# Kernel tuning notes

Measured on AMD Instinct MI355X. Metric: run time of the kernel, lower is better.

Reference implementation:

```python
import jax, jax.numpy as jnp
import numpy as np

B, C, H, W = 4, 512, 64, 64
IC = C // 2  # inter_plane
EPS = 1e-5


def _conv1x1(x, w, b=None):
    # x: [b,c,h,w], w: [o,c] -> [b,o,h,w]
    y = jnp.einsum('bchw,oc->bohw', x, w)
    if b is not None:
        y = y + b[None, :, None, None]
    return y


def setup_inputs() -> dict:
    key = jax.random.key(0)
    ks = jax.random.split(key, 20)
    rn = lambda i, sh, s=0.02: jax.random.normal(ks[i], sh, jnp.float32) * s
    return {
        'xA': jax.random.normal(ks[0], (B, C, H, W), jnp.float32),
        'wk': rn(1, (IC, C)), 'bk': rn(2, (IC,)),
        'wv': rn(3, (IC, C)), 'bv': rn(4, (IC,)),
        'wq': rn(5, (IC, C)), 'bq': rn(6, (IC,)),
        'wwg': rn(7, (IC, IC)),
        'bn1_g': jnp.ones((IC,), jnp.float32), 'bn1_b': rn(8, (IC,)),
        'bn1_m': rn(9, (IC,)), 'bn1_v': jax.random.uniform(ks[10], (IC,), jnp.float32, 0.5, 1.5),
        'wout': rn(11, (C, IC)), 'bout': rn(12, (C,)),
        'bn2_g': jnp.ones((C,), jnp.float32), 'bn2_b': rn(13, (C,)),
        'bn2_m': rn(14, (C,)), 'bn2_v': jax.random.uniform(ks[15], (C,), jnp.float32, 0.5, 1.5),
    }


def reference(xA, wk, bk, wv, bv, wq, bq, wwg, bn1_g, bn1_b, bn1_m, bn1_v,
              wout, bout, bn2_g, bn2_b, bn2_m, bn2_v):
    b, c, h, w = xA.shape
    n = h * w
    k = _conv1x1(xA, wk, bk).reshape(b, IC, n)   # [b,ic,n]
    v = _conv1x1(xA, wv, bv).reshape(b, IC, n)   # [b,ic,n] (permuted via einsum below)
    q = _conv1x1(xA, wq, bq).reshape(b, IC, n)   # [b,ic,n]
    # AV = softmax(v^T @ q, axis=2): [b,n,n]
    attn = jax.nn.softmax(jnp.einsum('bcn,bcm->bnm', v, q), axis=2)
    av = jnp.einsum('bcn,bnm->bcm', k, attn)     # [b,ic,n]
    # conv1d 1x1 (no bias) + BatchNorm1d (eval mode)
    avw = jnp.einsum('oc,bcn->bon', wwg, av)
    scale1 = bn1_g / jnp.sqrt(bn1_v + EPS)
    avw = (avw - bn1_m[None, :, None]) * scale1[None, :, None] + bn1_b[None, :, None]
    avw = avw.reshape(b, IC, h, w)
    # out conv + BatchNorm2d (eval) + residual + relu
    o = _conv1x1(avw, wout, bout)
    scale2 = bn2_g / jnp.sqrt(bn2_v + EPS)
    o = (o - bn2_m[None, :, None, None]) * scale2[None, :, None, None] + bn2_b[None, :, None, None]
    return jax.nn.relu(o + xA)
```

## Files before the change

### kernel.cpp

```cpp
#include <hip/hip_runtime.h>


#define N_ 4096
#define C_ 512
#define IC_ 256
#define B_ 4

typedef __bf16 bf16_t;
typedef __bf16 bf16x8 __attribute__((ext_vector_type(8)));
typedef __bf16 bf16x4 __attribute__((ext_vector_type(4)));
typedef float f32x4 __attribute__((ext_vector_type(4)));

#define GLD(g, l) __builtin_amdgcn_global_load_lds(                              \
    (const __attribute__((address_space(1))) void*)(g),                          \
    (__attribute__((address_space(3))) void*)(l), 16, 0, 0)

__device__ __forceinline__ void gemm_bt_128x128(
    const bf16_t* __restrict__ A, int lda,
    const bf16_t* __restrict__ Bt, int ldb,
    int K, int m0, int n0,
    bf16_t* smem, f32x4 acc[4][4])
{
    const int tid  = threadIdx.x;
    const int wave = tid >> 6, lane = tid & 63;
    const int wr = (wave >> 1) * 64, wc = (wave & 1) * 64;
    const int q = lane >> 4, l15 = lane & 15;
    const int srow = lane >> 3;
    const int scol = (((lane & 7) ^ (srow & 7)) * 8);
    const int swz  = l15 & 7;

#define GB_STAGE(bi, kt)                                                        \
    do {                                                                        \
        bf16_t* lA = smem + (bi) * 16384;                                       \
        bf16_t* lB = lA + 8192;                                                 \
        _Pragma("unroll")                                                       \
        for (int c = 0; c < 4; ++c) {                                           \
            const int ch = wave * 4 + c;                                        \
            GLD(A  + (size_t)(m0 + ch * 8 + srow) * lda + (kt) + scol,          \
                lA + ch * 512);                                                 \
            GLD(Bt + (size_t)(n0 + ch * 8 + srow) * ldb + (kt) + scol,          \
                lB + ch * 512);                                                 \
        }                                                                       \
    } while (0)

    GB_STAGE(0, 0);
    asm volatile("s_waitcnt vmcnt(0)" ::: "memory");
    __builtin_amdgcn_s_barrier();
    asm volatile("" ::: "memory");

    const int nt = K / 64;
    for (int t = 0; t < nt; ++t) {
        const int cur = t & 1;
        if (t + 1 < nt) GB_STAGE(cur ^ 1, (t + 1) * 64);
        const bf16_t* lsA = smem + cur * 16384;
        const bf16_t* lsB = lsA + 8192;
#pragma unroll
        for (int ks = 0; ks < 2; ++ks) {
            bf16x8 af[4], bfr[4];
            const int co = ((ks * 4 + q) ^ swz) * 8;
#pragma unroll
            for (int i = 0; i < 4; ++i) {
                af[i]  = *(const bf16x8*)&lsA[(wr + i * 16 + l15) * 64 + co];
                bfr[i] = *(const bf16x8*)&lsB[(wc + i * 16 + l15) * 64 + co];
            }
#pragma unroll
            for (int i = 0; i < 4; ++i)
#pragma unroll
                for (int j = 0; j < 4; ++j)
                    acc[i][j] = __builtin_amdgcn_mfma_f32_16x16x32_bf16(
                        af[i], bfr[j], acc[i][j], 0, 0, 0);
        }
        asm volatile("s_waitcnt vmcnt(0)" ::: "memory");
        __builtin_amdgcn_s_barrier();
        asm volatile("" ::: "memory");
    }
#undef GB_STAGE
}

#define ACC_ZERO(acc)                                                           \
    _Pragma("unroll") for (int i = 0; i < 4; ++i)                               \
    _Pragma("unroll") for (int j = 0; j < 4; ++j)                               \
        acc[i][j] = f32x4{0.f, 0.f, 0.f, 0.f};

__global__ __launch_bounds__(256) void prep_k(
    const float* __restrict__ wk, const float* __restrict__ wv,
    const float* __restrict__ wq,
    const float* __restrict__ wwg, const float* __restrict__ wout,
    const float* __restrict__ bout,
    const float* __restrict__ g1, const float* __restrict__ b1,
    const float* __restrict__ m1, const float* __restrict__ v1,
    const float* __restrict__ g2, const float* __restrict__ b2,
    const float* __restrict__ m2, const float* __restrict__ v2,
    bf16_t* __restrict__ Wb3, bf16_t* __restrict__ Wfb,
    float* __restrict__ bfv, float* __restrict__ rowsum)
{
    const int bid = blockIdx.x;
    __shared__ float ws[256];
    __shared__ float red[4];

    if (bid < 1536) {
        const int i = bid * 256 + threadIdx.x;
        float v;
        if      (i < 131072) v = wk[i];
        else if (i < 262144) v = wv[i - 131072];
        else                 v = wq[i - 262144];
        Wb3[i] = (bf16_t)v;
    } else if (bid < 2048) {
        const int o = bid - 1536;
        const int j = threadIdx.x;
        const float s1 = g1[j] * rsqrtf(v1[j] + 1e-5f);
        const float wo = wout[o * 256 + j];
        ws[j] = wo * s1;
        float bp = wo * (b1[j] - m1[j] * s1);
#pragma unroll
        for (int off = 32; off > 0; off >>= 1) bp += __shfl_down(bp, off);
        if ((j & 63) == 0) red[j >> 6] = bp;
        __syncthreads();

        float acc = 0.f;
#pragma unroll 4
        for (int ic = 0; ic < 256; ++ic)
            acc += ws[ic] * wwg[ic * 256 + j];

        const float s2 = g2[o] * rsqrtf(v2[o] + 1e-5f);
        Wfb[o * 256 + j] = (bf16_t)(acc * s2);
        if (j == 0)
            bfv[o] = s2 * (red[0] + red[1] + red[2] + red[3] + bout[o])
                     - s2 * m2[o] + b2[o];
    } else {
        rowsum[(bid - 2048) * 256 + threadIdx.x] = 0.f;
    }
}

__global__ __launch_bounds__(256) void txa_k(
    const float* __restrict__ xA, bf16_t* __restrict__ xAt)
{
    __shared__ float t[32][33];
    const int b = blockIdx.z;
    const int n0 = blockIdx.x * 32, c0 = blockIdx.y * 32;
    const int tx = threadIdx.x, ty = threadIdx.y;
    const float* X = xA + (size_t)b * C_ * N_;
    bf16_t* Y = xAt + (size_t)b * N_ * C_;
#pragma unroll
    for (int r = 0; r < 4; ++r)
        t[ty + r * 8][tx] = X[(size_t)(c0 + ty + r * 8) * N_ + n0 + tx];
    __syncthreads();
#pragma unroll
    for (int r = 0; r < 4; ++r)
        Y[(size_t)(n0 + ty + r * 8) * C_ + c0 + tx] = (bf16_t)t[tx][ty + r * 8];
}

__global__ __launch_bounds__(256) void conv_mfma_k(
    const bf16_t* __restrict__ Wb3,
    const float* __restrict__ bk, const float* __restrict__ bv,
    const float* __restrict__ bq, const bf16_t* __restrict__ xAt,
    bf16_t* __restrict__ Kb, bf16_t* __restrict__ Vt, bf16_t* __restrict__ Qt)
{
    __shared__ bf16_t smem[32768];
    const int which = blockIdx.z % 3, b = blockIdx.z / 3;
    const bf16_t* A = Wb3 + which * 131072;
    const float* bias = (which == 0) ? bk : (which == 1 ? bv : bq);
    const bf16_t* Bt = xAt + (size_t)b * N_ * C_;
    const int n0 = blockIdx.x * 128, m0 = blockIdx.y * 128;

    f32x4 acc[4][4];
    ACC_ZERO(acc);
    gemm_bt_128x128(A, C_, Bt, C_, C_, m0, n0, smem, acc);

    const int lane = threadIdx.x & 63, wave = threadIdx.x >> 6;
    const int q = lane >> 4, l15 = lane & 15;
    const int wr = (wave >> 1) * 64, wc = (wave & 1) * 64;

    if (which == 0) {
        bf16_t* Y = Kb + (size_t)b * IC_ * N_;
#pragma unroll
        for (int i = 0; i < 4; ++i)
#pragma unroll
            for (int r = 0; r < 4; ++r) {
                const int o = m0 + wr + i * 16 + q * 4 + r;
                const float bo = bias[o];
#pragma unroll
                for (int j = 0; j < 4; ++j)
                    Y[(size_t)o * N_ + n0 + wc + j * 16 + l15] =
                        (bf16_t)(acc[i][j][r] + bo);
            }
    } else {
        bf16_t* Y = ((which == 1) ? Vt : Qt) + (size_t)b * N_ * IC_;
#pragma unroll
        for (int i = 0; i < 4; ++i) {
            const int ob = m0 + wr + i * 16 + q * 4;
            float bo[4];
#pragma unroll
            for (int r = 0; r < 4; ++r) bo[r] = bias[ob + r];
#pragma unroll
            for (int j = 0; j < 4; ++j) {
                const int n = n0 + wc + j * 16 + l15;
                bf16x4 v4;
#pragma unroll
                for (int r = 0; r < 4; ++r) v4[r] = (bf16_t)(acc[i][j][r] + bo[r]);
                *(bf16x4*)&Y[(size_t)n * IC_ + ob] = v4;
            }
        }
    }
}

__global__ __launch_bounds__(512, 2) void s_mfma_t_k(
    const bf16_t* __restrict__ Qt, const bf16_t* __restrict__ Vt,
    bf16_t* __restrict__ Pt, float* __restrict__ rowsum)
{
    __shared__ bf16_t smem[49152];
    const int b  = blockIdx.z;
    const int n0 = blockIdx.x * 256;
    const int m0 = blockIdx.y * 256;
    const size_t NIC = (size_t)N_ * IC_;
    const bf16_t* Qb = Qt + (size_t)b * NIC;
    const bf16_t* Vb = Vt + (size_t)b * NIC;
    bf16_t* Pb = Pt + (size_t)b * N_ * N_;
    float* rs = rowsum + b * N_;

    const int tid  = threadIdx.x;
    const int wave = tid >> 6, lane = tid & 63;
    const int wr = wave >> 2;
    const int wn = wave & 3;
    const int q = lane >> 4, l15 = lane & 15;
    const int lr  = lane >> 2;
    const int swl = ((lane >> 2) & 3) ^ ((lane >> 4) & 3);
    const int sc8 = ((lane & 3) ^ swl) * 8;
    const int swr = (l15 & 3) ^ ((l15 >> 2) & 3);
    const int co  = (q ^ swr) * 8;

    f32x4 acc[8][4];
#pragma unroll
    for (int i = 0; i < 8; ++i)
#pragma unroll
        for (int j = 0; j < 4; ++j) acc[i][j] = f32x4{0.f, 0.f, 0.f, 0.f};

#define S_STAGE(buf, kt)                                                        \
    do {                                                                        \
        _Pragma("unroll")                                                       \
        for (int c = 0; c < 2; ++c) {                                           \
            const int ch = wave * 2 + c;                                        \
            const int gr = ch * 16 + lr;                                        \
            GLD(Qb + (size_t)(m0 + gr) * IC_ + (kt) + sc8, (buf) + ch * 512);   \
            GLD(Vb + (size_t)(n0 + gr) * IC_ + (kt) + sc8,                      \
                (buf) + 8192 + ch * 512);                                       \
        }                                                                       \
    } while (0)

    const int NT = IC_ / 32;
    S_STAGE(smem, 0);
    S_STAGE(smem + 16384, 32);

    int bc = 0, bs = 2;
    for (int t = 0; t < NT; ++t) {
        if (t + 1 < NT) {
            asm volatile("s_waitcnt vmcnt(4)" ::: "memory");
        } else {
            asm volatile("s_waitcnt vmcnt(0)" ::: "memory");
        }
        __builtin_amdgcn_s_barrier();
        asm volatile("" ::: "memory");
        if (t + 2 < NT) S_STAGE(smem + bs * 16384, (t + 2) * 32);

        const bf16_t* lsA = smem + bc * 16384;
        const bf16_t* lsB = lsA + 8192;
        bf16x8 af[8], bf[4];
#pragma unroll
        for (int i = 0; i < 8; ++i)
            af[i] = *(const bf16x8*)&lsA[(wr * 128 + i * 16 + l15) * 32 + co];
#pragma unroll
        for (int j = 0; j < 4; ++j)
            bf[j] = *(const bf16x8*)&lsB[(wn * 64 + j * 16 + l15) * 32 + co];
#pragma unroll
        for (int i = 0; i < 8; ++i)
#pragma unroll
            for (int j = 0; j < 4; ++j)
                acc[i][j] = __builtin_amdgcn_mfma_f32_16x16x32_bf16(
                    af[i], bf[j], acc[i][j], 0, 0, 0);
        bc = (bc == 2) ? 0 : bc + 1;
        bs = (bs == 2) ? 0 : bs + 1;
    }
#undef S_STAGE

#pragma unroll
    for (int h = 0; h < 2; ++h) {
        if ((wn >> 1) == h) {
#pragma unroll
            for (int j = 0; j < 4; ++j) {
                float cs = 0.f;
#pragma unroll
                for (int i = 0; i < 8; ++i)
#pragma unroll
                    for (int r = 0; r < 4; ++r) {
                        const float e = __expf(acc[i][j][r]);
                        cs += e;
                        smem[(wr * 128 + i * 16 + q * 4 + r) * 136 +
                             (wn & 1) * 64 + j * 16 + l15] = (bf16_t)e;
                    }
                cs += __shfl_xor(cs, 16);
                cs += __shfl_xor(cs, 32);
                if (q == 0) atomicAdd(&rs[n0 + wn * 64 + j * 16 + l15], cs);
            }
        }
        __syncthreads();
        const int rr0 = tid >> 4;
        const int cc  = (tid & 15) * 8;
#pragma unroll
        for (int pp = 0; pp < 8; ++pp) {
            const int rr = rr0 + pp * 32;
            const bf16x8 v = *(const bf16x8*)&smem[rr * 136 + cc];
            *(bf16x8*)&Pb[(size_t)(m0 + rr) * N_ + n0 + h * 128 + cc] = v;
        }
        __syncthreads();
    }
}

__global__ __launch_bounds__(256) void kscale_k(
    bf16_t* __restrict__ Kb, const float* __restrict__ rowsum)
{
    const size_t i8 = ((size_t)blockIdx.x * 256 + threadIdx.x) * 8;
    const int n = (int)(i8 & (N_ - 1));
    const int b = (int)(i8 >> 20);
    const float* rs = rowsum + b * N_;
    bf16x8 v = *(bf16x8*)&Kb[i8];
    const f32x4 r0 = *(const f32x4*)&rs[n];
    const f32x4 r1 = *(const f32x4*)&rs[n + 4];
#pragma unroll
    for (int k = 0; k < 4; ++k) {
        v[k]     = (bf16_t)((float)v[k]     / r0[k]);
        v[4 + k] = (bf16_t)((float)v[4 + k] / r1[k]);
    }
    *(bf16x8*)&Kb[i8] = v;
}

__global__ __launch_bounds__(256) void av_mfma_k(
    const bf16_t* __restrict__ Pt, const bf16_t* __restrict__ Kb,
    bf16_t* __restrict__ avTb)
{
    __shared__ bf16_t smem[3 * 16384];
    const int b  = blockIdx.z;
    const int m0 = blockIdx.x * 128;
    const int c0 = blockIdx.y * 128;
    const size_t NIC = (size_t)N_ * IC_;
    const bf16_t* Pb  = Pt + (size_t)b * N_ * N_ + (size_t)m0 * N_;
    const bf16_t* Kbb = Kb + (size_t)b * NIC + (size_t)c0 * N_;

    const int tid = threadIdx.x;
    const int wave = tid >> 6, lane = tid & 63;
    const int wr = (wave >> 1) * 64, wc = (wave & 1) * 64;
    const int q = lane >> 4, l15 = lane & 15;
    const int srow = lane >> 3;
    const int scol = (((lane & 7) ^ (srow & 7)) * 8);
    const int swz  = l15 & 7;

    f32x4 acc[4][4];
    ACC_ZERO(acc);

#define AV_STAGE(buf, kt)                                                       \
    do {                                                                        \
        _Pragma("unroll")                                                       \
        for (int c = 0; c < 4; ++c) {                                           \
            const int ch = wave * 4 + c;                                        \
            GLD(Pb  + (size_t)(ch * 8 + srow) * N_ + (kt) + scol,               \
                (buf) + ch * 512);                                              \
            GLD(Kbb + (size_t)(ch * 8 + srow) * N_ + (kt) + scol,               \
                (buf) + 8192 + ch * 512);                                       \
        }                                                                       \
    } while (0)

    const int NT = N_ / 64;
    AV_STAGE(smem, 0);
    AV_STAGE(smem + 16384, 64);

    int bi_c = 0;
    int bi_s = 2;
    for (int t = 0; t < NT; ++t) {
        if (t + 2 < NT) {
            asm volatile("s_waitcnt vmcnt(8)" ::: "memory");
            __builtin_amdgcn_s_barrier();
            asm volatile("" ::: "memory");
            AV_STAGE(smem + bi_s * 16384, (t + 2) * 64);
        } else {
            asm volatile("s_waitcnt vmcnt(0)" ::: "memory");
            __builtin_amdgcn_s_barrier();
            asm volatile("" ::: "memory");
        }
        const bf16_t* lsA = smem + bi_c * 16384;
        const bf16_t* lsB = lsA + 8192;
#pragma unroll
        for (int ks = 0; ks < 2; ++ks) {
            const int co2 = ((ks * 4 + q) ^ swz) * 8;
            bf16x8 af[4], bfr[4];
#pragma unroll
            for (int i = 0; i < 4; ++i) {
                af[i]  = *(const bf16x8*)&lsA[(wr + i * 16 + l15) * 64 + co2];
                bfr[i] = *(const bf16x8*)&lsB[(wc + i * 16 + l15) * 64 + co2];
            }
#pragma unroll
            for (int i = 0; i < 4; ++i)
#pragma unroll
                for (int j = 0; j < 4; ++j)
                    acc[i][j] = __builtin_amdgcn_mfma_f32_16x16x32_bf16(
                        af[i], bfr[j], acc[i][j], 0, 0, 0);
        }
        bi_c = (bi_c == 2) ? 0 : bi_c + 1;
        bi_s = (bi_s == 2) ? 0 : bi_s + 1;
    }
#undef AV_STAGE
    __syncthreads();

#pragma unroll
    for (int i = 0; i < 4; ++i)
#pragma unroll
        for (int j = 0; j < 4; ++j)
#pragma unroll
            for (int r = 0; r < 4; ++r)
                smem[(wr + i * 16 + q * 4 + r) * 136 + wc + j * 16 + l15] =
                    (bf16_t)acc[i][j][r];
    __syncthreads();

    bf16_t* Y = avTb + (size_t)b * NIC + (size_t)m0 * IC_ + c0;
    const int rr = tid >> 4;
    const int cc = (tid & 15) * 8;
#pragma unroll
    for (int p = 0; p < 8; ++p) {
        const int mm = rr + p * 16;
        const bf16x8 v = *(const bf16x8*)&smem[mm * 136 + cc];
        *(bf16x8*)&Y[(size_t)mm * IC_ + cc] = v;
    }
}

__global__ __launch_bounds__(256) void out_mfma_k(
    const bf16_t* __restrict__ Wfb, const float* __restrict__ bfv,
    const bf16_t* __restrict__ avTb,
    const float* __restrict__ xA, float* __restrict__ out)
{
    __shared__ bf16_t smem[32768];
    const int b = blockIdx.z;
    const bf16_t* Bt = avTb + (size_t)b * N_ * IC_;
    const int n0 = blockIdx.x * 128, o0 = blockIdx.y * 128;

    f32x4 acc[4][4];
    ACC_ZERO(acc);
    gemm_bt_128x128(Wfb, IC_, Bt, IC_, IC_, o0, n0, smem, acc);

    const int lane = threadIdx.x & 63, wave = threadIdx.x >> 6;
    const int q = lane >> 4, l15 = lane & 15;
    const int wr = (wave >> 1) * 64, wc = (wave & 1) * 64;

#pragma unroll
    for (int i = 0; i < 4; ++i)
#pragma unroll
        for (int r = 0; r < 4; ++r) {
            const int o = o0 + wr + i * 16 + q * 4 + r;
            const float bo = bfv[o];
#pragma unroll
            for (int j = 0; j < 4; ++j) {
                const int n = n0 + wc + j * 16 + l15;
                const size_t idx = ((size_t)b * C_ + o) * N_ + n;
                out[idx] = fmaxf(acc[i][j][r] + bo + xA[idx], 0.f);
            }
        }
}

extern "C" void kernel_launch(void* const* d_in, const int* in_sizes, int n_in,
                              void* d_out, int out_size, void* d_ws, size_t ws_size,
                              hipStream_t stream)
{
    const float* xA    = (const float*)d_in[0];
    const float* wk    = (const float*)d_in[1];
    const float* bk    = (const float*)d_in[2];
    const float* wv    = (const float*)d_in[3];
    const float* bv    = (const float*)d_in[4];
    const float* wq    = (const float*)d_in[5];
    const float* bq    = (const float*)d_in[6];
    const float* wwg   = (const float*)d_in[7];
    const float* bn1_g = (const float*)d_in[8];
    const float* bn1_b = (const float*)d_in[9];
    const float* bn1_m = (const float*)d_in[10];
    const float* bn1_v = (const float*)d_in[11];
    const float* wout  = (const float*)d_in[12];
    const float* bout  = (const float*)d_in[13];
    const float* bn2_g = (const float*)d_in[14];
    const float* bn2_b = (const float*)d_in[15];
    const float* bn2_m = (const float*)d_in[16];
    const float* bn2_v = (const float*)d_in[17];
    float* out = (float*)d_out;

    char* p = (char*)d_ws;
    bf16_t* Wb3    = (bf16_t*)p; p += 786432;
    bf16_t* Wfb    = (bf16_t*)p; p += 262144;
    float*  bfv    = (float*)p;  p += 2048;
    bf16_t* xAt    = (bf16_t*)p;
    bf16_t* avTb   = (bf16_t*)p; p += 16777216;
    bf16_t* Kb     = (bf16_t*)p; p += 8388608;
    bf16_t* Vt     = (bf16_t*)p; p += 8388608;
    bf16_t* Qt     = (bf16_t*)p; p += 8388608;
    float*  rowsum = (float*)p;  p += 65536;
    bf16_t* Pt     = (bf16_t*)p; p += 134217728;

    prep_k<<<2112, 256, 0, stream>>>(wk, wv, wq, wwg, wout, bout,
                                     bn1_g, bn1_b, bn1_m, bn1_v,
                                     bn2_g, bn2_b, bn2_m, bn2_v,
                                     Wb3, Wfb, bfv, rowsum);
    txa_k<<<dim3(N_ / 32, C_ / 32, B_), dim3(32, 8), 0, stream>>>(xA, xAt);
    conv_mfma_k<<<dim3(N_ / 128, IC_ / 128, 3 * B_), 256, 0, stream>>>(
        Wb3, bk, bv, bq, xAt, Kb, Vt, Qt);

    s_mfma_t_k<<<dim3(N_ / 256, N_ / 256, B_), 512, 0, stream>>>(
        Qt, Vt, Pt, rowsum);
    kscale_k<<<2048, 256, 0, stream>>>(Kb, rowsum);
    av_mfma_k<<<dim3(N_ / 128, IC_ / 128, B_), 256, 0, stream>>>(Pt, Kb, avTb);

    out_mfma_k<<<dim3(N_ / 128, C_ / 128, B_), 256, 0, stream>>>(
        Wfb, bfv, avTb, xA, out);
}
```

Baseline: 289.5 us.

## Switch S-GEMM staging to double-buffered 64-wide K tiles with new swizzle

The score GEMM kernel now stages K tiles of 64 instead of 32 and uses two LDS buffers instead of a three-stage ring. The LDS swizzle changes to an 8-way XOR pattern on 64-element rows. The goal is fewer barriers and loop iterations per block. In exchange, LDS grows to 128 KB per block, which may reduce occupancy under launch_bounds(512,2), and there is less prefetch depth.

```diff
diff --git a/kernel.cpp b/kernel.cpp
--- a/kernel.cpp
+++ b/kernel.cpp
@@ -208,7 +208,7 @@
     const bf16_t* __restrict__ Qt, const bf16_t* __restrict__ Vt,
     bf16_t* __restrict__ Pt, float* __restrict__ rowsum)
 {
-    __shared__ bf16_t smem[49152];
+    __shared__ bf16_t smem[65536];
     const int b  = blockIdx.z;
     const int n0 = blockIdx.x * 256;
     const int m0 = blockIdx.y * 256;
@@ -223,11 +223,9 @@
     const int wr = wave >> 2;
     const int wn = wave & 3;
     const int q = lane >> 4, l15 = lane & 15;
-    const int lr  = lane >> 2;
-    const int swl = ((lane >> 2) & 3) ^ ((lane >> 4) & 3);
-    const int sc8 = ((lane & 3) ^ swl) * 8;
-    const int swr = (l15 & 3) ^ ((l15 >> 2) & 3);
-    const int co  = (q ^ swr) * 8;
+    const int srow = lane >> 3;
+    const int scol = (((lane & 7) ^ (srow & 7)) * 8);
+    const int swz  = l15 & 7;
 
     f32x4 acc[8][4];
 #pragma unroll
@@ -235,50 +233,51 @@
 #pragma unroll
         for (int j = 0; j < 4; ++j) acc[i][j] = f32x4{0.f, 0.f, 0.f, 0.f};
 
-#define S_STAGE(buf, kt)                                                        \
+#define S_STAGE(bi, kt)                                                         \
     do {                                                                        \
+        bf16_t* lA = smem + (bi) * 32768;                                       \
+        bf16_t* lB = lA + 16384;                                                \
         _Pragma("unroll")                                                       \
-        for (int c = 0; c < 2; ++c) {                                           \
-            const int ch = wave * 2 + c;                                        \
-            const int gr = ch * 16 + lr;                                        \
-            GLD(Qb + (size_t)(m0 + gr) * IC_ + (kt) + sc8, (buf) + ch * 512);   \
-            GLD(Vb + (size_t)(n0 + gr) * IC_ + (kt) + sc8,                      \
-                (buf) + 8192 + ch * 512);                                       \
+        for (int c = 0; c < 4; ++c) {                                           \
+            const int ch = wave * 4 + c;                                        \
+            GLD(Qb + (size_t)(m0 + ch * 8 + srow) * IC_ + (kt) + scol,          \
+                lA + ch * 512);                                                 \
+            GLD(Vb + (size_t)(n0 + ch * 8 + srow) * IC_ + (kt) + scol,          \
+                lB + ch * 512);                                                 \
         }                                                                       \
     } while (0)
 
-    const int NT = IC_ / 32;
-    S_STAGE(smem, 0);
-    S_STAGE(smem + 16384, 32);
-
-    int bc = 0, bs = 2;
+    S_STAGE(0, 0);
+    asm volatile("s_waitcnt vmcnt(0)" ::: "memory");
+    __builtin_amdgcn_s_barrier();
+    asm volatile("" ::: "memory");
+
+    const int NT = IC_ / 64;
     for (int t = 0; t < NT; ++t) {
-        if (t + 1 < NT) {
-            asm volatile("s_waitcnt vmcnt(4)" ::: "memory");
-        } else {
-            asm volatile("s_waitcnt vmcnt(0)" ::: "memory");
-        }
+        const int cur = t & 1;
+        if (t + 1 < NT) S_STAGE(cur ^ 1, (t + 1) * 64);
+        const bf16_t* lsA = smem + cur * 32768;
+        const bf16_t* lsB = lsA + 16384;
+#pragma unroll
+        for (int ks = 0; ks < 2; ++ks) {
+            const int co = ((ks * 4 + q) ^ swz) * 8;
+            bf16x8 af[8], bfv_[4];
+#pragma unroll
+            for (int i = 0; i < 8; ++i)
+                af[i] = *(const bf16x8*)&lsA[(wr * 128 + i * 16 + l15) * 64 + co];
+#pragma unroll
+            for (int j = 0; j < 4; ++j)
+                bfv_[j] = *(const bf16x8*)&lsB[(wn * 64 + j * 16 + l15) * 64 + co];
+#pragma unroll
+            for (int i = 0; i < 8; ++i)
+#pragma unroll
+                for (int j = 0; j < 4; ++j)
+                    acc[i][j] = __builtin_amdgcn_mfma_f32_16x16x32_bf16(
+                        af[i], bfv_[j], acc[i][j], 0, 0, 0);
+        }
+        asm volatile("s_waitcnt vmcnt(0)" ::: "memory");
         __builtin_amdgcn_s_barrier();
         asm volatile("" ::: "memory");
-        if (t + 2 < NT) S_STAGE(smem + bs * 16384, (t + 2) * 32);
-
-        const bf16_t* lsA = smem + bc * 16384;
-        const bf16_t* lsB = lsA + 8192;
-        bf16x8 af[8], bf[4];
-#pragma unroll
-        for (int i = 0; i < 8; ++i)
-            af[i] = *(const bf16x8*)&lsA[(wr * 128 + i * 16 + l15) * 32 + co];
-#pragma unroll
-        for (int j = 0; j < 4; ++j)
-            bf[j] = *(const bf16x8*)&lsB[(wn * 64 + j * 16 + l15) * 32 + co];
-#pragma unroll
-        for (int i = 0; i < 8; ++i)
-#pragma unroll
-            for (int j = 0; j < 4; ++j)
-                acc[i][j] = __builtin_amdgcn_mfma_f32_16x16x32_bf16(
-                    af[i], bf[j], acc[i][j], 0, 0, 0);
-        bc = (bc == 2) ? 0 : bc + 1;
-        bs = (bs == 2) ? 0 : bs + 1;
     }
 #undef S_STAGE
 
```

Result: no change. 287.5 us (-0.7%).
